# Kernel tuning notes

Hardware: AMD Instinct MI355X
Metric: run time of the kernel (lower is better)

The kernel has to match this reference:

```python
import jax, jax.numpy as jnp
import numpy as np

D_MODEL, D_STATE, D_CONV, EXPAND, D_FF = 1024, 16, 4, 2, 4096
D_INNER = D_MODEL * EXPAND
DT_MIN, DT_MAX = 0.001, 0.1
B_SZ, SEQ = 2, 1024


def setup_inputs() -> dict:
    key = jax.random.key(0)
    ks = jax.random.split(key, 24)
    s = 0.02
    return {
        "x": jax.random.normal(ks[0], (B_SZ, SEQ, D_MODEL), jnp.float32),
        "ln1_g": jnp.ones((D_MODEL,), jnp.float32),
        "ln1_b": jnp.zeros((D_MODEL,), jnp.float32),
        "W_in": jax.random.normal(ks[1], (D_MODEL, 2 * D_INNER), jnp.float32) * s,
        "b_in": jnp.zeros((2 * D_INNER,), jnp.float32),
        "conv_w": jax.random.normal(ks[2], (D_INNER, 1, D_CONV), jnp.float32) * s,
        "conv_b": jnp.zeros((D_INNER,), jnp.float32),
        "A_log": jax.random.normal(ks[3], (D_INNER, D_STATE), jnp.float32),
        "W_B": jax.random.normal(ks[4], (D_INNER, D_INNER * D_STATE), jnp.float32) * s,
        "b_B": jnp.zeros((D_INNER * D_STATE,), jnp.float32),
        "W_C": jax.random.normal(ks[5], (D_INNER, D_INNER * D_STATE), jnp.float32) * s,
        "b_C": jnp.zeros((D_INNER * D_STATE,), jnp.float32),
        "Dp": jnp.ones((D_INNER,), jnp.float32),
        "W_dt": jax.random.normal(ks[6], (D_INNER, D_INNER), jnp.float32) * s,
        "b_dt": jnp.zeros((D_INNER,), jnp.float32),
        "W_out": jax.random.normal(ks[7], (D_INNER, D_MODEL), jnp.float32) * s,
        "b_out": jnp.zeros((D_MODEL,), jnp.float32),
        "ln2_g": jnp.ones((D_MODEL,), jnp.float32),
        "ln2_b": jnp.zeros((D_MODEL,), jnp.float32),
        "W1": jax.random.normal(ks[8], (D_MODEL, D_FF), jnp.float32) * s,
        "b1": jnp.zeros((D_FF,), jnp.float32),
        "W2": jax.random.normal(ks[9], (D_FF, D_MODEL), jnp.float32) * s,
        "b2": jnp.zeros((D_MODEL,), jnp.float32),
    }


def _layernorm(x, g, b, eps=1e-5):
    m = jnp.mean(x, -1, keepdims=True)
    v = jnp.mean((x - m) ** 2, -1, keepdims=True)
    return (x - m) * jax.lax.rsqrt(v + eps) * g + b


def reference(x, ln1_g, ln1_b, W_in, b_in, conv_w, conv_b, A_log, W_B, b_B,
              W_C, b_C, Dp, W_dt, b_dt, W_out, b_out, ln2_g, ln2_b, W1, b1, W2, b2):
    B, S, _ = x.shape
    residual = x
    xn = _layernorm(x, ln1_g, ln1_b)
    xg = xn @ W_in + b_in                      # [B,S,2*D_INNER]
    x_proj, gate = jnp.split(xg, 2, axis=-1)   # each [B,S,D_INNER]
    # causal depthwise conv (pad left d_conv-1, truncate to S)
    xc = jax.lax.conv_general_dilated(
        x_proj.transpose(0, 2, 1), conv_w, window_strides=(1,),
        padding=[(D_CONV - 1, 0)], feature_group_count=D_INNER,
        dimension_numbers=("NCH", "OIH", "NCH")) + conv_b[None, :, None]
    xc = xc.transpose(0, 2, 1)                 # [B,S,D_INNER]
    delta = jax.nn.sigmoid(xc @ W_dt + b_dt) * (DT_MAX - DT_MIN) + DT_MIN
    A = -jnp.exp(A_log)                        # [D_INNER,D_STATE]
    A_bar = jnp.exp(delta[..., None] * A)      # [B,S,D_INNER,D_STATE]
    Bm = (xc @ W_B + b_B).reshape(B, S, D_INNER, D_STATE)
    Cm = (xc @ W_C + b_C).reshape(B, S, D_INNER, D_STATE)
    B_bar = delta[..., None] * Bm

    def step(h, ins):
        a, bb, xp_t, c = ins
        h = a * h + bb * xp_t[..., None]
        y = jnp.sum(c * h, -1)
        return h, y

    xs = (A_bar.transpose(1, 0, 2, 3), B_bar.transpose(1, 0, 2, 3),
          x_proj.transpose(1, 0, 2), Cm.transpose(1, 0, 2, 3))
    h0 = jnp.zeros((B, D_INNER, D_STATE), x.dtype)
    _, ys = jax.lax.scan(step, h0, xs)
    y = ys.transpose(1, 0, 2) + Dp * x_proj    # [B,S,D_INNER]
    y = y * jax.nn.silu(gate)
    x2 = residual + (y @ W_out + b_out)
    xn2 = _layernorm(x2, ln2_g, ln2_b)
    h1 = jax.nn.gelu(xn2 @ W1 + b1, approximate=False)
    return x2 + (h1 @ W2 + b2)
```

## Files before the change

### kernel.cpp

```cpp
#include <hip/hip_runtime.h>

typedef __bf16 bf16;
typedef __bf16 bf16x8 __attribute__((ext_vector_type(8)));
typedef float f32x4 __attribute__((ext_vector_type(4)));

#define D_MODEL 1024
#define D_STATE 16
#define D_CONV 4
#define D_INNER 2048
#define D_FF 4096
#define B_SZ 2
#define SEQ 1024
#define NTOK (B_SZ * SEQ)
#define NCHUNK 16
#define CLEN (SEQ / NCHUNK)

__global__ __launch_bounds__(256) void ln_kernel(const float* __restrict__ x,
                                                 const float* __restrict__ g,
                                                 const float* __restrict__ b,
                                                 bf16* __restrict__ out) {
  int row = blockIdx.x;
  const float* xr = x + (size_t)row * D_MODEL;
  int t = threadIdx.x;
  float4 v = ((const float4*)xr)[t];
  float s = v.x + v.y + v.z + v.w;
  float s2 = v.x * v.x + v.y * v.y + v.z * v.z + v.w * v.w;
  for (int off = 32; off > 0; off >>= 1) {
    s += __shfl_down(s, off);
    s2 += __shfl_down(s2, off);
  }
  __shared__ float red[8];
  int wid = t >> 6, lane = t & 63;
  if (lane == 0) { red[wid] = s; red[4 + wid] = s2; }
  __syncthreads();
  if (t == 0) {
    float a = red[0] + red[1] + red[2] + red[3];
    float a2 = red[4] + red[5] + red[6] + red[7];
    red[0] = a * (1.0f / D_MODEL);
    red[1] = a2 * (1.0f / D_MODEL);
  }
  __syncthreads();
  float mean = red[0];
  float var = red[1] - mean * mean;
  float rs = rsqrtf(var + 1e-5f);
  float4 gg = ((const float4*)g)[t];
  float4 bb = ((const float4*)b)[t];
  bf16 o[4] __attribute__((aligned(8)));
  o[0] = (bf16)((v.x - mean) * rs * gg.x + bb.x);
  o[1] = (bf16)((v.y - mean) * rs * gg.y + bb.y);
  o[2] = (bf16)((v.z - mean) * rs * gg.z + bb.z);
  o[3] = (bf16)((v.w - mean) * rs * gg.w + bb.w);
  *(uint2*)&out[(size_t)row * D_MODEL + t * 4] = *(const uint2*)o;
}

__global__ __launch_bounds__(256) void transpose_bf16_kernel(
    const float* __restrict__ W, bf16* __restrict__ Wt, int K, int N) {
  __shared__ float tile[32][33];
  int n0 = blockIdx.x * 32, k0 = blockIdx.y * 32;
  int t = threadIdx.x;
  int kr = t >> 3;
  int nc = (t & 7) * 4;
  float4 v = *(const float4*)&W[(size_t)(k0 + kr) * N + n0 + nc];
  tile[kr][nc + 0] = v.x;
  tile[kr][nc + 1] = v.y;
  tile[kr][nc + 2] = v.z;
  tile[kr][nc + 3] = v.w;
  __syncthreads();
  int nr = t >> 3;
  int kc = (t & 7) * 4;
  bf16 o[4] __attribute__((aligned(8)));
  o[0] = (bf16)tile[kc + 0][nr];
  o[1] = (bf16)tile[kc + 1][nr];
  o[2] = (bf16)tile[kc + 2][nr];
  o[3] = (bf16)tile[kc + 3][nr];
  *(uint2*)&Wt[(size_t)(n0 + nr) * K + k0 + kc] = *(const uint2*)o;
}

__global__ __launch_bounds__(256) void conv_kernel(const float* __restrict__ xg,
                                                   const float* __restrict__ cw,
                                                   const float* __restrict__ cb,
                                                   bf16* __restrict__ xc) {
  int idx = blockIdx.x * 256 + threadIdx.x;
  int d = idx & (D_INNER - 1);
  int s = (idx >> 11) & (SEQ - 1);
  int b = idx >> 21;
  const float* base = xg + (size_t)b * SEQ * (2 * D_INNER);
  float acc = cb[d];
#pragma unroll
  for (int j = 0; j < 4; j++) {
    int sp = s - 3 + j;
    if (sp >= 0) acc += base[(size_t)sp * (2 * D_INNER) + d] * cw[d * 4 + j];
  }
  xc[idx] = (bf16)acc;
}


__global__ __launch_bounds__(256) void scan_phase1(
    const bf16* __restrict__ Bm, const float* __restrict__ delta,
    const float* __restrict__ xg, const float* __restrict__ A_log,
    float* __restrict__ Pprod, float* __restrict__ Hloc) {
  int tid = blockIdx.x * 256 + threadIdx.x;
  int n = tid & 15;
  int d = (tid >> 4) & (D_INNER - 1);
  int c = (tid >> 15) & (NCHUNK - 1);
  int b = tid >> 19;
  float A = -__expf(A_log[d * D_STATE + n]);
  int s0 = c * CLEN;
  size_t bc = ((size_t)(b * SEQ + s0) * D_INNER + d) * D_STATE + n;
  size_t dB = (size_t)(b * SEQ + s0) * D_INNER + d;
  size_t gB = (size_t)(b * SEQ + s0) * (2 * D_INNER) + d;
  float h = 0.f, P = 1.f;
  for (int s = 0; s < CLEN; s++) {
    float bm = (float)Bm[bc + (size_t)s * (D_INNER * D_STATE)];
    float dl = delta[dB + (size_t)s * D_INNER];
    float xp = xg[gB + (size_t)s * (2 * D_INNER)];
    float a = __expf(dl * A);
    h = a * h + (dl * bm) * xp;
    P *= a;
  }
  size_t o = ((size_t)((b * NCHUNK + c) * D_INNER) + d) * D_STATE + n;
  Pprod[o] = P;
  Hloc[o] = h;
}

__global__ __launch_bounds__(256) void scan_phase2(
    const float* __restrict__ Pprod, const float* __restrict__ Hloc,
    float* __restrict__ Hstart) {
  int tid = blockIdx.x * 256 + threadIdx.x;
  int n = tid & 15;
  int d = (tid >> 4) & (D_INNER - 1);
  int b = tid >> 15;
  float h = 0.f;
#pragma unroll
  for (int c = 0; c < NCHUNK; c++) {
    size_t o = ((size_t)((b * NCHUNK + c) * D_INNER) + d) * D_STATE + n;
    Hstart[o] = h;
    h = Pprod[o] * h + Hloc[o];
  }
}

__global__ __launch_bounds__(256) void scan_phase3(
    const bf16* __restrict__ Bm, const bf16* __restrict__ Cm,
    const float* __restrict__ delta, const float* __restrict__ xg,
    const float* __restrict__ A_log, const float* __restrict__ Dp,
    const float* __restrict__ Hstart, bf16* __restrict__ y) {
  int tid = blockIdx.x * 256 + threadIdx.x;
  int n = tid & 15;
  int d = (tid >> 4) & (D_INNER - 1);
  int c = (tid >> 15) & (NCHUNK - 1);
  int b = tid >> 19;
  float A = -__expf(A_log[d * D_STATE + n]);
  float dcoef = Dp[d];
  int s0 = c * CLEN;
  size_t bc = ((size_t)(b * SEQ + s0) * D_INNER + d) * D_STATE + n;
  size_t dB = (size_t)(b * SEQ + s0) * D_INNER + d;
  size_t gB = (size_t)(b * SEQ + s0) * (2 * D_INNER) + d;
  float h = Hstart[((size_t)((b * NCHUNK + c) * D_INNER) + d) * D_STATE + n];
  for (int s = 0; s < CLEN; s++) {
    float bm = (float)Bm[bc + (size_t)s * (D_INNER * D_STATE)];
    float cm = (float)Cm[bc + (size_t)s * (D_INNER * D_STATE)];
    float dl = delta[dB + (size_t)s * D_INNER];
    float xp = xg[gB + (size_t)s * (2 * D_INNER)];
    float a = __expf(dl * A);
    h = a * h + (dl * bm) * xp;
    float p = cm * h;
    p += __shfl_xor(p, 1);
    p += __shfl_xor(p, 2);
    p += __shfl_xor(p, 4);
    p += __shfl_xor(p, 8);
    if (n == 0) {
      float gt = xg[gB + D_INNER + (size_t)s * (2 * D_INNER)];
      float sig = 1.f / (1.f + __expf(-gt));
      float yv = (p + dcoef * xp) * (gt * sig);
      y[dB + (size_t)s * D_INNER] = (bf16)yv;
    }
  }
}

enum { EPI_PLAIN = 0, EPI_DT = 1, EPI_BF16 = 2, EPI_ADD = 3, EPI_GELU = 4 };

template <int EPI>
__global__ __launch_bounds__(256) void gemm_bf16(
    const bf16* __restrict__ A, const bf16* __restrict__ Bt,
    const float* __restrict__ bias, const float* __restrict__ extra,
    void* __restrict__ outv, int M, int N, int K) {
  __shared__ bf16 As[128 * 40];
  __shared__ bf16 Bs[128 * 40];
  int t = threadIdx.x;
  int lane = t & 63, wid = t >> 6;
  int wm = wid & 1, wn = wid >> 1;
  int l16 = lane & 15, quad = lane >> 4;
  int m0 = blockIdx.y * 128, n0 = blockIdx.x * 128;

  int srow = t >> 1, shalf = t & 1;
  const uint4* ga = (const uint4*)(A + (size_t)(m0 + srow) * K) + shalf * 2;
  const uint4* gb = (const uint4*)(Bt + (size_t)(n0 + srow) * K) + shalf * 2;
  uint4* la = (uint4*)&As[srow * 40 + shalf * 16];
  uint4* lb = (uint4*)&Bs[srow * 40 + shalf * 16];

  f32x4 acc[4][4] = {};
  for (int k0 = 0; k0 < K; k0 += 32) {
    uint4 a0 = ga[0], a1 = ga[1];
    uint4 b0 = gb[0], b1 = gb[1];
    __syncthreads();
    la[0] = a0; la[1] = a1;
    lb[0] = b0; lb[1] = b1;
    __syncthreads();
    bf16x8 af[4], bfr[4];
#pragma unroll
    for (int i = 0; i < 4; i++) {
      af[i]  = *(const bf16x8*)&As[(wm * 64 + i * 16 + l16) * 40 + quad * 8];
      bfr[i] = *(const bf16x8*)&Bs[(wn * 64 + i * 16 + l16) * 40 + quad * 8];
    }
#pragma unroll
    for (int mi = 0; mi < 4; mi++)
#pragma unroll
      for (int ni = 0; ni < 4; ni++)
        acc[mi][ni] = __builtin_amdgcn_mfma_f32_16x16x32_bf16(af[mi], bfr[ni],
                                                              acc[mi][ni], 0, 0, 0);
    ga += 4;
    gb += 4;
  }
#pragma unroll
  for (int mi = 0; mi < 4; mi++) {
#pragma unroll
    for (int ni = 0; ni < 4; ni++) {
      int col = n0 + wn * 64 + ni * 16 + l16;
      int mrow0 = m0 + wm * 64 + mi * 16 + quad * 4;
#pragma unroll
      for (int r = 0; r < 4; r++) {
        int m = mrow0 + r;
        float v = acc[mi][ni][r] + bias[col];
        size_t o = (size_t)m * N + col;
        if (EPI == EPI_PLAIN) {
          ((float*)outv)[o] = v;
        } else if (EPI == EPI_DT) {
          ((float*)outv)[o] = (1.f / (1.f + __expf(-v))) * 0.099f + 0.001f;
        } else if (EPI == EPI_BF16) {
          ((bf16*)outv)[o] = (bf16)v;
        } else if (EPI == EPI_ADD) {
          ((float*)outv)[o] = v + extra[o];
        } else if (EPI == EPI_GELU) {
          ((bf16*)outv)[o] = (bf16)(0.5f * v * (1.f + erff(v * 0.70710678118f)));
        }
      }
    }
  }
}

extern "C" void kernel_launch(void* const* d_in, const int* in_sizes, int n_in,
                              void* d_out, int out_size, void* d_ws, size_t ws_size,
                              hipStream_t stream) {
  const float* x      = (const float*)d_in[0];
  const float* ln1_g  = (const float*)d_in[1];
  const float* ln1_b  = (const float*)d_in[2];
  const float* W_in   = (const float*)d_in[3];
  const float* b_in   = (const float*)d_in[4];
  const float* conv_w = (const float*)d_in[5];
  const float* conv_b = (const float*)d_in[6];
  const float* A_log  = (const float*)d_in[7];
  const float* W_B    = (const float*)d_in[8];
  const float* b_B    = (const float*)d_in[9];
  const float* W_C    = (const float*)d_in[10];
  const float* b_C    = (const float*)d_in[11];
  const float* Dp     = (const float*)d_in[12];
  const float* W_dt   = (const float*)d_in[13];
  const float* b_dt   = (const float*)d_in[14];
  const float* W_out  = (const float*)d_in[15];
  const float* b_out  = (const float*)d_in[16];
  const float* ln2_g  = (const float*)d_in[17];
  const float* ln2_b  = (const float*)d_in[18];
  const float* W1     = (const float*)d_in[19];
  const float* b1     = (const float*)d_in[20];
  const float* W2     = (const float*)d_in[21];
  const float* b2     = (const float*)d_in[22];
  float* out = (float*)d_out;

  char* ws = (char*)d_ws;
  size_t off = 0;
  auto alloc = [&](size_t bytes) -> void* {
    void* p = ws + off;
    off += (bytes + 255) & ~(size_t)255;
    return p;
  };
  bf16*  xn_bf  = (bf16*)alloc((size_t)NTOK * D_MODEL * 2);
  float* xg     = (float*)alloc((size_t)NTOK * 2 * D_INNER * 4);
  bf16*  xc_bf  = (bf16*)alloc((size_t)NTOK * D_INNER * 2);
  float* delta  = (float*)alloc((size_t)NTOK * D_INNER * 4);
  bf16*  Bm     = (bf16*)alloc((size_t)NTOK * D_INNER * D_STATE * 2);
  bf16*  Cm     = (bf16*)alloc((size_t)NTOK * D_INNER * D_STATE * 2);
  bf16*  y_bf   = (bf16*)alloc((size_t)NTOK * D_INNER * 2);
  float* x2     = (float*)alloc((size_t)NTOK * D_MODEL * 4);
  bf16*  xn2_bf = (bf16*)alloc((size_t)NTOK * D_MODEL * 2);
  bf16*  h1_bf  = (bf16*)alloc((size_t)NTOK * D_FF * 2);
  float* Pprod  = (float*)alloc((size_t)B_SZ * NCHUNK * D_INNER * D_STATE * 4);
  float* Hloc   = (float*)alloc((size_t)B_SZ * NCHUNK * D_INNER * D_STATE * 4);
  float* Hstart = (float*)alloc((size_t)B_SZ * NCHUNK * D_INNER * D_STATE * 4);
  bf16*  wt     = (bf16*)alloc((size_t)D_INNER * (D_INNER * D_STATE) * 2);

  dim3 blk(256);

  ln_kernel<<<NTOK, blk, 0, stream>>>(x, ln1_g, ln1_b, xn_bf);
  transpose_bf16_kernel<<<dim3((2 * D_INNER) / 32, D_MODEL / 32), blk, 0, stream>>>(
      W_in, wt, D_MODEL, 2 * D_INNER);
  gemm_bf16<EPI_PLAIN><<<dim3((2 * D_INNER) / 128, NTOK / 128), blk, 0, stream>>>(
      xn_bf, wt, b_in, nullptr, xg, NTOK, 2 * D_INNER, D_MODEL);
  conv_kernel<<<(NTOK * D_INNER) / 256, blk, 0, stream>>>(xg, conv_w, conv_b, xc_bf);
  transpose_bf16_kernel<<<dim3(D_INNER / 32, D_INNER / 32), blk, 0, stream>>>(
      W_dt, wt, D_INNER, D_INNER);
  gemm_bf16<EPI_DT><<<dim3(D_INNER / 128, NTOK / 128), blk, 0, stream>>>(
      xc_bf, wt, b_dt, nullptr, delta, NTOK, D_INNER, D_INNER);
  transpose_bf16_kernel<<<dim3((D_INNER * D_STATE) / 32, D_INNER / 32), blk, 0, stream>>>(
      W_B, wt, D_INNER, D_INNER * D_STATE);
  gemm_bf16<EPI_BF16><<<dim3((D_INNER * D_STATE) / 128, NTOK / 128), blk, 0, stream>>>(
      xc_bf, wt, b_B, nullptr, Bm, NTOK, D_INNER * D_STATE, D_INNER);
  transpose_bf16_kernel<<<dim3((D_INNER * D_STATE) / 32, D_INNER / 32), blk, 0, stream>>>(
      W_C, wt, D_INNER, D_INNER * D_STATE);
  gemm_bf16<EPI_BF16><<<dim3((D_INNER * D_STATE) / 128, NTOK / 128), blk, 0, stream>>>(
      xc_bf, wt, b_C, nullptr, Cm, NTOK, D_INNER * D_STATE, D_INNER);
  scan_phase1<<<(B_SZ * NCHUNK * D_INNER * D_STATE) / 256, blk, 0, stream>>>(
      Bm, delta, xg, A_log, Pprod, Hloc);
  scan_phase2<<<(B_SZ * D_INNER * D_STATE) / 256, blk, 0, stream>>>(
      Pprod, Hloc, Hstart);
  scan_phase3<<<(B_SZ * NCHUNK * D_INNER * D_STATE) / 256, blk, 0, stream>>>(
      Bm, Cm, delta, xg, A_log, Dp, Hstart, y_bf);
  transpose_bf16_kernel<<<dim3(D_MODEL / 32, D_INNER / 32), blk, 0, stream>>>(
      W_out, wt, D_INNER, D_MODEL);
  gemm_bf16<EPI_ADD><<<dim3(D_MODEL / 128, NTOK / 128), blk, 0, stream>>>(
      y_bf, wt, b_out, x, x2, NTOK, D_MODEL, D_INNER);
  ln_kernel<<<NTOK, blk, 0, stream>>>(x2, ln2_g, ln2_b, xn2_bf);
  transpose_bf16_kernel<<<dim3(D_FF / 32, D_MODEL / 32), blk, 0, stream>>>(
      W1, wt, D_MODEL, D_FF);
  gemm_bf16<EPI_GELU><<<dim3(D_FF / 128, NTOK / 128), blk, 0, stream>>>(
      xn2_bf, wt, b1, nullptr, h1_bf, NTOK, D_FF, D_MODEL);
  transpose_bf16_kernel<<<dim3(D_MODEL / 32, D_FF / 32), blk, 0, stream>>>(
      W2, wt, D_FF, D_MODEL);
  gemm_bf16<EPI_ADD><<<dim3(D_MODEL / 128, NTOK / 128), blk, 0, stream>>>(
      h1_bf, wt, b2, x2, out, NTOK, D_MODEL, D_FF);
}
```

Before: 1.999 ms.

## Use direct global-to-LDS loads in GEMM, widen transpose tiles, swap grid order

The GEMM now stages A and B tiles through global_load_lds, which copies global memory straight into shared memory without going through registers, and drops the padded LDS row stride. The weight transpose kernel moves to 64x64 tiles and writes 16-byte bf16 vectors. The GEMM grid is reordered so blockIdx.x walks M, so consecutive blocks share the same weight columns, which is meant to improve L2 reuse of the large weight matrices. Removing the padding risks LDS bank conflicts on the MFMA fragment reads, and there is no register prefetch to overlap loads with compute.

```diff
diff --git a/kernel.cpp b/kernel.cpp
--- a/kernel.cpp
+++ b/kernel.cpp
@@ -14,6 +14,11 @@
 #define NTOK (B_SZ * SEQ)
 #define NCHUNK 16
 #define CLEN (SEQ / NCHUNK)
+
+#define GLOAD_LDS16(gptr, ldsptr)                                            \
+  __builtin_amdgcn_global_load_lds(                                          \
+      (const __attribute__((address_space(1))) unsigned int*)(gptr),         \
+      (__attribute__((address_space(3))) unsigned int*)(ldsptr), 16, 0, 0)
 
 __global__ __launch_bounds__(256) void ln_kernel(const float* __restrict__ x,
                                                  const float* __restrict__ g,
@@ -55,25 +60,30 @@
 
 __global__ __launch_bounds__(256) void transpose_bf16_kernel(
     const float* __restrict__ W, bf16* __restrict__ Wt, int K, int N) {
-  __shared__ float tile[32][33];
-  int n0 = blockIdx.x * 32, k0 = blockIdx.y * 32;
+  __shared__ float tile[64][65];
+  int n0 = blockIdx.x * 64, k0 = blockIdx.y * 64;
   int t = threadIdx.x;
-  int kr = t >> 3;
-  int nc = (t & 7) * 4;
-  float4 v = *(const float4*)&W[(size_t)(k0 + kr) * N + n0 + nc];
-  tile[kr][nc + 0] = v.x;
-  tile[kr][nc + 1] = v.y;
-  tile[kr][nc + 2] = v.z;
-  tile[kr][nc + 3] = v.w;
+  int kr = t >> 4;
+  int nc = (t & 15) * 4;
+#pragma unroll
+  for (int g = 0; g < 4; g++) {
+    float4 v = *(const float4*)&W[(size_t)(k0 + kr + g * 16) * N + n0 + nc];
+    tile[kr + g * 16][nc + 0] = v.x;
+    tile[kr + g * 16][nc + 1] = v.y;
+    tile[kr + g * 16][nc + 2] = v.z;
+    tile[kr + g * 16][nc + 3] = v.w;
+  }
   __syncthreads();
   int nr = t >> 3;
-  int kc = (t & 7) * 4;
-  bf16 o[4] __attribute__((aligned(8)));
-  o[0] = (bf16)tile[kc + 0][nr];
-  o[1] = (bf16)tile[kc + 1][nr];
-  o[2] = (bf16)tile[kc + 2][nr];
-  o[3] = (bf16)tile[kc + 3][nr];
-  *(uint2*)&Wt[(size_t)(n0 + nr) * K + k0 + kc] = *(const uint2*)o;
+  int kc = (t & 7) * 8;
+#pragma unroll
+  for (int p = 0; p < 2; p++) {
+    int n = nr + p * 32;
+    bf16 o[8] __attribute__((aligned(16)));
+#pragma unroll
+    for (int i = 0; i < 8; i++) o[i] = (bf16)tile[kc + i][n];
+    *(uint4*)&Wt[(size_t)(n0 + n) * K + k0 + kc] = *(const uint4*)o;
+  }
 }
 
 __global__ __launch_bounds__(256) void conv_kernel(const float* __restrict__ xg,
@@ -93,7 +103,6 @@
   }
   xc[idx] = (bf16)acc;
 }
-
 
 __global__ __launch_bounds__(256) void scan_phase1(
     const bf16* __restrict__ Bm, const float* __restrict__ delta,
@@ -184,33 +193,38 @@
     const bf16* __restrict__ A, const bf16* __restrict__ Bt,
     const float* __restrict__ bias, const float* __restrict__ extra,
     void* __restrict__ outv, int M, int N, int K) {
-  __shared__ bf16 As[128 * 40];
-  __shared__ bf16 Bs[128 * 40];
+  __shared__ bf16 As[128 * 32];
+  __shared__ bf16 Bs[128 * 32];
   int t = threadIdx.x;
   int lane = t & 63, wid = t >> 6;
   int wm = wid & 1, wn = wid >> 1;
   int l16 = lane & 15, quad = lane >> 4;
-  int m0 = blockIdx.y * 128, n0 = blockIdx.x * 128;
-
-  int srow = t >> 1, shalf = t & 1;
-  const uint4* ga = (const uint4*)(A + (size_t)(m0 + srow) * K) + shalf * 2;
-  const uint4* gb = (const uint4*)(Bt + (size_t)(n0 + srow) * K) + shalf * 2;
-  uint4* la = (uint4*)&As[srow * 40 + shalf * 16];
-  uint4* lb = (uint4*)&Bs[srow * 40 + shalf * 16];
+  int m0 = blockIdx.x * 128, n0 = blockIdx.y * 128;
+
+  int srow = wid * 16 + (lane >> 2);
+  int scol = (lane & 3) * 8;
+  const bf16* ga0 = A + (size_t)(m0 + srow) * K + scol;
+  const bf16* ga1 = ga0 + (size_t)64 * K;
+  const bf16* gb0 = Bt + (size_t)(n0 + srow) * K + scol;
+  const bf16* gb1 = gb0 + (size_t)64 * K;
+  bf16* lA0 = &As[wid * 512];
+  bf16* lA1 = &As[2048 + wid * 512];
+  bf16* lB0 = &Bs[wid * 512];
+  bf16* lB1 = &Bs[2048 + wid * 512];
 
   f32x4 acc[4][4] = {};
   for (int k0 = 0; k0 < K; k0 += 32) {
-    uint4 a0 = ga[0], a1 = ga[1];
-    uint4 b0 = gb[0], b1 = gb[1];
     __syncthreads();
-    la[0] = a0; la[1] = a1;
-    lb[0] = b0; lb[1] = b1;
+    GLOAD_LDS16(ga0 + k0, lA0);
+    GLOAD_LDS16(ga1 + k0, lA1);
+    GLOAD_LDS16(gb0 + k0, lB0);
+    GLOAD_LDS16(gb1 + k0, lB1);
     __syncthreads();
     bf16x8 af[4], bfr[4];
 #pragma unroll
     for (int i = 0; i < 4; i++) {
-      af[i]  = *(const bf16x8*)&As[(wm * 64 + i * 16 + l16) * 40 + quad * 8];
-      bfr[i] = *(const bf16x8*)&Bs[(wn * 64 + i * 16 + l16) * 40 + quad * 8];
+      af[i]  = *(const bf16x8*)&As[(wm * 64 + i * 16 + l16) * 32 + quad * 8];
+      bfr[i] = *(const bf16x8*)&Bs[(wn * 64 + i * 16 + l16) * 32 + quad * 8];
     }
 #pragma unroll
     for (int mi = 0; mi < 4; mi++)
@@ -218,8 +232,6 @@
       for (int ni = 0; ni < 4; ni++)
         acc[mi][ni] = __builtin_amdgcn_mfma_f32_16x16x32_bf16(af[mi], bfr[ni],
                                                               acc[mi][ni], 0, 0, 0);
-    ga += 4;
-    gb += 4;
   }
 #pragma unroll
   for (int mi = 0; mi < 4; mi++) {
@@ -301,22 +313,22 @@
   dim3 blk(256);
 
   ln_kernel<<<NTOK, blk, 0, stream>>>(x, ln1_g, ln1_b, xn_bf);
-  transpose_bf16_kernel<<<dim3((2 * D_INNER) / 32, D_MODEL / 32), blk, 0, stream>>>(
+  transpose_bf16_kernel<<<dim3((2 * D_INNER) / 64, D_MODEL / 64), blk, 0, stream>>>(
       W_in, wt, D_MODEL, 2 * D_INNER);
-  gemm_bf16<EPI_PLAIN><<<dim3((2 * D_INNER) / 128, NTOK / 128), blk, 0, stream>>>(
+  gemm_bf16<EPI_PLAIN><<<dim3(NTOK / 128, (2 * D_INNER) / 128), blk, 0, stream>>>(
       xn_bf, wt, b_in, nullptr, xg, NTOK, 2 * D_INNER, D_MODEL);
   conv_kernel<<<(NTOK * D_INNER) / 256, blk, 0, stream>>>(xg, conv_w, conv_b, xc_bf);
-  transpose_bf16_kernel<<<dim3(D_INNER / 32, D_INNER / 32), blk, 0, stream>>>(
+  transpose_bf16_kernel<<<dim3(D_INNER / 64, D_INNER / 64), blk, 0, stream>>>(
       W_dt, wt, D_INNER, D_INNER);
-  gemm_bf16<EPI_DT><<<dim3(D_INNER / 128, NTOK / 128), blk, 0, stream>>>(
+  gemm_bf16<EPI_DT><<<dim3(NTOK / 128, D_INNER / 128), blk, 0, stream>>>(
       xc_bf, wt, b_dt, nullptr, delta, NTOK, D_INNER, D_INNER);
-  transpose_bf16_kernel<<<dim3((D_INNER * D_STATE) / 32, D_INNER / 32), blk, 0, stream>>>(
+  transpose_bf16_kernel<<<dim3((D_INNER * D_STATE) / 64, D_INNER / 64), blk, 0, stream>>>(
       W_B, wt, D_INNER, D_INNER * D_STATE);
-  gemm_bf16<EPI_BF16><<<dim3((D_INNER * D_STATE) / 128, NTOK / 128), blk, 0, stream>>>(
+  gemm_bf16<EPI_BF16><<<dim3(NTOK / 128, (D_INNER * D_STATE) / 128), blk, 0, stream>>>(
       xc_bf, wt, b_B, nullptr, Bm, NTOK, D_INNER * D_STATE, D_INNER);
-  transpose_bf16_kernel<<<dim3((D_INNER * D_STATE) / 32, D_INNER / 32), blk, 0, stream>>>(
+  transpose_bf16_kernel<<<dim3((D_INNER * D_STATE) / 64, D_INNER / 64), blk, 0, stream>>>(
       W_C, wt, D_INNER, D_INNER * D_STATE);
-  gemm_bf16<EPI_BF16><<<dim3((D_INNER * D_STATE) / 128, NTOK / 128), blk, 0, stream>>>(
+  gemm_bf16<EPI_BF16><<<dim3(NTOK / 128, (D_INNER * D_STATE) / 128), blk, 0, stream>>>(
       xc_bf, wt, b_C, nullptr, Cm, NTOK, D_INNER * D_STATE, D_INNER);
   scan_phase1<<<(B_SZ * NCHUNK * D_INNER * D_STATE) / 256, blk, 0, stream>>>(
       Bm, delta, xg, A_log, Pprod, Hloc);
@@ -324,17 +336,17 @@
       Pprod, Hloc, Hstart);
   scan_phase3<<<(B_SZ * NCHUNK * D_INNER * D_STATE) / 256, blk, 0, stream>>>(
       Bm, Cm, delta, xg, A_log, Dp, Hstart, y_bf);
-  transpose_bf16_kernel<<<dim3(D_MODEL / 32, D_INNER / 32), blk, 0, stream>>>(
+  transpose_bf16_kernel<<<dim3(D_MODEL / 64, D_INNER / 64), blk, 0, stream>>>(
       W_out, wt, D_INNER, D_MODEL);
-  gemm_bf16<EPI_ADD><<<dim3(D_MODEL / 128, NTOK / 128), blk, 0, stream>>>(
+  gemm_bf16<EPI_ADD><<<dim3(NTOK / 128, D_MODEL / 128), blk, 0, stream>>>(
       y_bf, wt, b_out, x, x2, NTOK, D_MODEL, D_INNER);
   ln_kernel<<<NTOK, blk, 0, stream>>>(x2, ln2_g, ln2_b, xn2_bf);
-  transpose_bf16_kernel<<<dim3(D_FF / 32, D_MODEL / 32), blk, 0, stream>>>(
+  transpose_bf16_kernel<<<dim3(D_FF / 64, D_MODEL / 64), blk, 0, stream>>>(
       W1, wt, D_MODEL, D_FF);
-  gemm_bf16<EPI_GELU><<<dim3(D_FF / 128, NTOK / 128), blk, 0, stream>>>(
+  gemm_bf16<EPI_GELU><<<dim3(NTOK / 128, D_FF / 128), blk, 0, stream>>>(
       xn2_bf, wt, b1, nullptr, h1_bf, NTOK, D_FF, D_MODEL);
-  transpose_bf16_kernel<<<dim3(D_MODEL / 32, D_FF / 32), blk, 0, stream>>>(
+  transpose_bf16_kernel<<<dim3(D_MODEL / 64, D_FF / 64), blk, 0, stream>>>(
       W2, wt, D_FF, D_MODEL);
-  gemm_bf16<EPI_ADD><<<dim3(D_MODEL / 128, NTOK / 128), blk, 0, stream>>>(
+  gemm_bf16<EPI_ADD><<<dim3(NTOK / 128, D_MODEL / 128), blk, 0, stream>>>(
       h1_bf, wt, b2, x2, out, NTOK, D_MODEL, D_FF);
 }
```

New measurement: 1.884 ms. -5.7%, faster.
